# Kernel tuning notes

Measured on AMD Instinct MI355X. Metric: run time of the kernel, lower is better.

The kernel has to match this reference:

```python
import jax, jax.numpy as jnp
import numpy as np
from jax import lax

B, CIN, COUT, H, W = 16, 256, 128, 32, 32
KD = 3   # deformable conv kernel
KU = 4
PAD = 1  # deform conv padding
EPS = 1e-5


def setup_inputs() -> dict:
    key = jax.random.key(0)
    ks = jax.random.split(key, 5)
    s3 = 1.0 / np.sqrt(CIN * KD * KD)
    s_up = 1.0 / np.sqrt(COUT * KU * KU)
    return {
        "x": jax.random.normal(ks[0], (B, CIN, H, W), jnp.float32),
        "w_off": jax.random.normal(ks[1], (3 * KD * KD, CIN, KD, KD), jnp.float32) * s3,
        "b_off": jnp.zeros((3 * KD * KD,), jnp.float32),
        "w_dcn": jax.random.normal(ks[2], (COUT, CIN, KD, KD), jnp.float32) * s3,
        "b_dcn": jnp.zeros((COUT,), jnp.float32),
        "g1": jnp.ones((COUT,), jnp.float32),
        "bt1": jnp.zeros((COUT,), jnp.float32),
        "w_up": jax.random.normal(ks[3], (COUT, COUT, KU, KU), jnp.float32) * s_up,  # torch ConvTranspose2d weight layout (in, out, kh, kw)
        "g2": jnp.ones((COUT,), jnp.float32),
        "bt2": jnp.zeros((COUT,), jnp.float32),
    }


def _conv3x3(x, w, b):
    y = lax.conv_general_dilated(x, w, (1, 1), [(1, 1), (1, 1)],
                                 dimension_numbers=("NCHW", "OIHW", "NCHW"))
    return y + b[None, :, None, None]


def _bn_relu(x, g, b):
    # training-mode BatchNorm2d: batch stats over (N, H, W), biased variance
    mu = jnp.mean(x, (0, 2, 3), keepdims=True)
    var = jnp.var(x, (0, 2, 3), keepdims=True)
    y = (x - mu) * lax.rsqrt(var + EPS)
    return jax.nn.relu(y * g[None, :, None, None] + b[None, :, None, None])


def _deform_conv(x, offset, mask, w, b):
    # modulated deformable conv v2, matching torchvision.ops.DeformConv2d
    Bb, C, Hh, Ww = x.shape
    Kk = KD * KD
    off = offset.reshape(Bb, Kk, 2, Hh, Ww)
    dy, dx = off[:, :, 0], off[:, :, 1]          # [B, Kk, H, W]
    ky, kx = jnp.meshgrid(jnp.arange(KD), jnp.arange(KD), indexing="ij")
    ky = (ky.reshape(-1) - PAD).astype(x.dtype)  # [Kk]
    kx = (kx.reshape(-1) - PAD).astype(x.dtype)
    ii = jnp.arange(Hh, dtype=x.dtype)[None, None, :, None]
    jj = jnp.arange(Ww, dtype=x.dtype)[None, None, None, :]
    py = ii + ky[None, :, None, None] + dy       # [B, Kk, H, W] sample rows
    px = jj + kx[None, :, None, None] + dx       # [B, Kk, H, W] sample cols
    y0 = jnp.floor(py)
    x0 = jnp.floor(px)
    wy = py - y0
    wx = px - x0
    HW = Hh * Ww
    x_flat = x.reshape(Bb, 1, C, HW)

    def corner(yc, xc, wgt):
        valid = (yc >= 0) & (yc <= Hh - 1) & (xc >= 0) & (xc <= Ww - 1)
        yi = jnp.clip(yc, 0, Hh - 1).astype(jnp.int32)
        xi = jnp.clip(xc, 0, Ww - 1).astype(jnp.int32)
        idx = (yi * Ww + xi).reshape(Bb, Kk, 1, HW)
        v = jnp.take_along_axis(x_flat, jnp.broadcast_to(idx, (Bb, Kk, C, HW)), axis=-1)
        wv = (wgt * valid.astype(x.dtype)).reshape(Bb, Kk, 1, HW)
        return v * wv

    samp = (corner(y0, x0, (1 - wy) * (1 - wx)) + corner(y0, x0 + 1, (1 - wy) * wx)
            + corner(y0 + 1, x0, wy * (1 - wx)) + corner(y0 + 1, x0 + 1, wy * wx))
    samp = samp * mask.reshape(Bb, Kk, 1, HW)    # [B, Kk, C, HW]
    out = jnp.einsum("bkcp,ock->bop", samp, w.reshape(w.shape[0], C, Kk))
    return out.reshape(Bb, -1, Hh, Ww) + b[None, :, None, None]


def reference(x, w_off, b_off, w_dcn, b_dcn, g1, bt1, w_up, g2, bt2):
    off = _conv3x3(x, w_off, b_off)              # [B, 27, H, W]
    Kk = KD * KD
    o1, o2, m = off[:, :Kk], off[:, Kk:2 * Kk], off[:, 2 * Kk:]
    offset = jnp.concatenate([o1, o2], axis=1)   # [B, 18, H, W], torchvision pair layout
    mask = jax.nn.sigmoid(m)
    y = _deform_conv(x, offset, mask, w_dcn, b_dcn)
    y = _bn_relu(y, g1, bt1)
    # ConvTranspose2d(k=4, s=2, p=1): conv over lhs-dilated input with flipped kernel
    w_t = jnp.flip(w_up, (2, 3)).transpose(1, 0, 2, 3)  # (out, in, kh, kw)
    p = KU - 1 - 1  # k - 1 - deconv_pad
    y = lax.conv_general_dilated(y, w_t, (1, 1), [(p, p), (p, p)],
                                 lhs_dilation=(2, 2),
                                 dimension_numbers=("NCHW", "OIHW", "NCHW"))
    return _bn_relu(y, g2, bt2)
```

## Files before the change

kernel.cpp:

```cpp
#include <hip/hip_runtime.h>
#include <hip/hip_fp16.h>
#include <math.h>

#define HW 1024
#define EPSV 1e-5f

typedef unsigned int uint;
typedef unsigned short ushort;
typedef __attribute__((ext_vector_type(8))) short short8;
typedef __attribute__((ext_vector_type(8))) _Float16 half8;
typedef __attribute__((ext_vector_type(4))) float floatx4;

static const size_t BOFF = 0;
static const size_t BD   = 36864;
static const size_t BQ   = 184320;
static const size_t XT   = 315392;
static const size_t OFFB = 2412544;
static const size_t ST1  = 2936832;
static const size_t ST2  = 2937856;
static const size_t YP   = 2941952;
static const size_t YSUM = 7136256;
static const size_t YBN  = 8184832;
static const size_t OB   = 9233408;

__device__ inline ushort f2bf(float f) {
  uint u = __builtin_bit_cast(uint, f);
  uint r = (u + 0x7FFFu + ((u >> 16) & 1u)) >> 16;
  return (ushort)r;
}
__device__ inline float b2f(ushort u) {
  return __builtin_bit_cast(float, ((uint)u) << 16);
}

__global__ __launch_bounds__(256) void prep_xt_kernel(const float* __restrict__ x,
                                                      const float* __restrict__ w_off,
                                                      const float* __restrict__ w_dcn,
                                                      const float* __restrict__ w_up,
                                                      float* __restrict__ ws) {
  __shared__ float tile[64 * 65];
  int blk = blockIdx.x;
  int tid = threadIdx.x;
  if (blk < 1024) {
    int b = blk & 15, pt = (blk >> 4) & 15, cc = blk >> 8;
    int p0 = pt * 64, c0 = cc * 64;
    int pp4 = tid & 15, ci = tid >> 4;
#pragma unroll
    for (int it = 0; it < 4; ++it) {
      int c = it * 16 + ci;
      float4 v = *(const float4*)(x + ((size_t)(b * 256 + c0 + c)) * HW + p0 + pp4 * 4);
      tile[c * 65 + pp4 * 4 + 0] = v.x;
      tile[c * 65 + pp4 * 4 + 1] = v.y;
      tile[c * 65 + pp4 * 4 + 2] = v.z;
      tile[c * 65 + pp4 * 4 + 3] = v.w;
    }
    __syncthreads();
    int cp = tid & 31, pp2 = tid >> 5;
    uint* xtu = (uint*)(ws + XT);
#pragma unroll
    for (int it = 0; it < 8; ++it) {
      int p = it * 8 + pp2;
      __half2 h = __floats2half2_rn(tile[(2 * cp) * 65 + p], tile[(2 * cp + 1) * 65 + p]);
      xtu[(size_t)(b * 1024 + p0 + p) * 128 + cc * 32 + cp] = __builtin_bit_cast(uint, h);
    }
  } else if (blk < 3488) {
    int i = (blk - 1024) * 256 + tid;
    if (i < 73728) {
      int c = i & 255; int n = (i >> 8) & 31; int tap = i >> 13;
      float v = (n < 27) ? w_off[((size_t)n * 256 + c) * 9 + tap] : 0.f;
      ((__half*)(ws + BOFF))[i] = __float2half(v);
    } else if (i < 73728 + 294912) {
      int d = i - 73728;
      int oc = d / 2304; int k = d % 2304;
      int tap = k >> 8; int c = k & 255;
      ((__half*)(ws + BD))[d] = __float2half(w_dcn[((size_t)oc * 256 + c) * 9 + tap]);
    } else if (i < 73728 + 294912 + 262144) {
      int d = i - (73728 + 294912);
      int j = d & 7; int n = (d >> 3) & 127; int quad = (d >> 10) & 3;
      int kstep = (d >> 12) & 15; int par = d >> 16;
      int k = kstep * 32 + quad * 8 + j;
      int t4 = k >> 7; int c = k & 127;
      int ty = t4 >> 1, tx = t4 & 1;
      int pu = par >> 1, pv = par & 1;
      int ky = (1 - pu) + 2 * ty, kx = (1 - pv) + 2 * tx;
      float v = w_up[((size_t)c * 128 + n) * 16 + ky * 4 + kx];
      ((ushort*)(ws + BQ))[d] = f2bf(v);
    }
  } else {
    int i = (blk - 3488) * 256 + tid;
    if (i < 5120) ws[ST1 + i] = 0.f;
    else if (i < 5120 + 524288) ws[OFFB + (i - 5120)] = 0.f;
  }
}

__global__ __launch_bounds__(256) void offconv_mfma_kernel(const __half* __restrict__ xt,
                                                           const __half* __restrict__ boff,
                                                           float* __restrict__ off) {
  __shared__ short As[32 * 132];
  __shared__ short Bs[32 * 132];
  int blk = blockIdx.x;
  int b = blk & 15, cs = (blk >> 4) & 1, pt = blk >> 5;
  int P0 = pt * 32;
  int tid = threadIdx.x;
  int wid = tid >> 6, lane = tid & 63, lr = lane & 15, quad = lane >> 4;
  int m_w = (wid & 1) * 16, n_w = (wid >> 1) * 16;
  int arow = tid >> 3, aseg = tid & 7;
  int pix = P0 + arow; int h = pix >> 5, w = pix & 31;

  floatx4 acc = (floatx4)0.f;

  for (int tap = 0; tap < 9; ++tap) {
    int ty = tap / 3, tx = tap % 3;
    int yy = h + ty - 1, xx = w + tx - 1;
    bool valid = (yy >= 0) && (yy < 32) && (xx >= 0) && (xx < 32);
    int pos = min(max(yy, 0), 31) * 32 + min(max(xx, 0), 31);
    const float4* ga = (const float4*)(xt + ((size_t)(b * 1024 + pos)) * 256 + cs * 128 + aseg * 16);
    float4 a0 = ga[0], a1 = ga[1];
    if (!valid) { a0 = make_float4(0.f, 0.f, 0.f, 0.f); a1 = a0; }
    const float4* gb = (const float4*)(boff + ((size_t)(tap * 32 + arow)) * 256 + cs * 128 + aseg * 16);
    float4 b0 = gb[0], b1 = gb[1];
    if (tap) __syncthreads();
    float4* qa = (float4*)(As + arow * 132 + aseg * 16);
    qa[0] = a0; qa[1] = a1;
    float4* qb = (float4*)(Bs + arow * 132 + aseg * 16);
    qb[0] = b0; qb[1] = b1;
    __syncthreads();
#pragma unroll
    for (int k2 = 0; k2 < 4; ++k2) {
      half8 af = *(const half8*)(As + (m_w + lr) * 132 + k2 * 32 + quad * 8);
      half8 bf = *(const half8*)(Bs + (n_w + lr) * 132 + k2 * 32 + quad * 8);
      acc = __builtin_amdgcn_mfma_f32_16x16x32_f16(af, bf, acc, 0, 0, 0);
    }
  }
  int n = n_w + lr;
#pragma unroll
  for (int r = 0; r < 4; ++r) {
    int m = m_w + quad * 4 + r;
    atomicAdd(&off[((size_t)(b * 1024 + P0 + m)) * 32 + n], acc[r]);
  }
}

__global__ __launch_bounds__(256) void deform_mfma_kernel(const __half* __restrict__ xt,
                                                          const float* __restrict__ off,
                                                          const float* __restrict__ b_off,
                                                          const __half* __restrict__ bd,
                                                          ushort* __restrict__ y_part) {
  __shared__ short As[64 * 72];
  __shared__ short Bs[128 * 72];
  int blk = blockIdx.x;
  int b = blk & 15;
  int rr = blk >> 4;
  int ptile = rr & 15, cs = rr >> 4;
  int tid = threadIdx.x;
  int wid = tid >> 6, lane = tid & 63, lr = lane & 15, quad = lane >> 4;
  int m_w = (wid & 1) * 32, n_w = (wid >> 1) * 64;
  int P0 = ptile * 64;
  int pix_l = tid >> 2, cseg = tid & 3;
  int pix = P0 + pix_l;
  int h = pix >> 5, w = pix & 31;
  const float* offb = off + (size_t)(b * 1024 + pix) * 32;
  const __half* xb = xt + (size_t)b * 1024 * 256 + cs * 64 + cseg * 16;
  int ocb = tid >> 1, seg = tid & 1;
  const __half* bdr = bd + (size_t)ocb * 2304 + cs * 64 + seg * 32;

  float4 o4[7];
#pragma unroll
  for (int i = 0; i < 7; ++i) o4[i] = ((const float4*)offb)[i];
  float oflat[28];
#pragma unroll
  for (int i = 0; i < 7; ++i) {
    oflat[4 * i] = o4[i].x; oflat[4 * i + 1] = o4[i].y;
    oflat[4 * i + 2] = o4[i].z; oflat[4 * i + 3] = o4[i].w;
  }

  floatx4 acc[2][4];
#pragma unroll
  for (int mi = 0; mi < 2; ++mi)
#pragma unroll
    for (int ni = 0; ni < 4; ++ni) acc[mi][ni] = (floatx4)0.f;

#pragma unroll
  for (int tap = 0; tap < 9; ++tap) {
    float dy = oflat[2 * tap] + b_off[2 * tap];
    float dx = oflat[2 * tap + 1] + b_off[2 * tap + 1];
    float mraw = oflat[18 + tap] + b_off[18 + tap];
    float mm = 1.f / (1.f + __expf(-mraw));
    float py = (float)(h + tap / 3 - 1) + dy;
    float px = (float)(w + tap % 3 - 1) + dx;
    float y0f = floorf(py), x0f = floorf(px);
    float wy = py - y0f, wx = px - x0f;
    int y0 = (int)y0f, x0 = (int)x0f;
    float cw[4] = {(1.f - wy) * (1.f - wx), (1.f - wy) * wx, wy * (1.f - wx), wy * wx};
    uint4 q[4][2];
    __half2 w2[4];
#pragma unroll
    for (int t = 0; t < 4; ++t) {
      int yy = y0 + (t >> 1), xx = x0 + (t & 1);
      bool v = (yy >= 0) && (yy <= 31) && (xx >= 0) && (xx <= 31);
      int yc = min(max(yy, 0), 31), xc = min(max(xx, 0), 31);
      const uint4* xr = (const uint4*)(xb + (size_t)(yc * 32 + xc) * 256);
      q[t][0] = xr[0]; q[t][1] = xr[1];
      w2[t] = __float2half2_rn(v ? cw[t] * mm : 0.f);
    }
    const float4* gb = (const float4*)(bdr + tap * 256);
    float4 b0 = gb[0], b1 = gb[1], b2 = gb[2], b3 = gb[3];

    __half2 hacc[8];
#pragma unroll
    for (int j = 0; j < 8; ++j) hacc[j] = __float2half2_rn(0.f);
#pragma unroll
    for (int t = 0; t < 4; ++t) {
      uint qa[8] = {q[t][0].x, q[t][0].y, q[t][0].z, q[t][0].w,
                    q[t][1].x, q[t][1].y, q[t][1].z, q[t][1].w};
#pragma unroll
      for (int j = 0; j < 8; ++j)
        hacc[j] = __hfma2(w2[t], __builtin_bit_cast(__half2, qa[j]), hacc[j]);
    }
    if (tap) __syncthreads();
    {
      float4 f0, f1;
      f0.x = __builtin_bit_cast(float, hacc[0]);
      f0.y = __builtin_bit_cast(float, hacc[1]);
      f0.z = __builtin_bit_cast(float, hacc[2]);
      f0.w = __builtin_bit_cast(float, hacc[3]);
      f1.x = __builtin_bit_cast(float, hacc[4]);
      f1.y = __builtin_bit_cast(float, hacc[5]);
      f1.z = __builtin_bit_cast(float, hacc[6]);
      f1.w = __builtin_bit_cast(float, hacc[7]);
      float4* qa2 = (float4*)(As + pix_l * 72 + cseg * 16);
      qa2[0] = f0; qa2[1] = f1;
    }
    float4* qb = (float4*)(Bs + ocb * 72 + seg * 32);
    qb[0] = b0; qb[1] = b1; qb[2] = b2; qb[3] = b3;
    __syncthreads();
#pragma unroll
    for (int k2 = 0; k2 < 2; ++k2) {
      half8 af[2], bf[4];
#pragma unroll
      for (int mi = 0; mi < 2; ++mi)
        af[mi] = *(const half8*)(As + (m_w + mi * 16 + lr) * 72 + k2 * 32 + quad * 8);
#pragma unroll
      for (int ni = 0; ni < 4; ++ni)
        bf[ni] = *(const half8*)(Bs + (n_w + ni * 16 + lr) * 72 + k2 * 32 + quad * 8);
#pragma unroll
      for (int mi = 0; mi < 2; ++mi)
#pragma unroll
        for (int ni = 0; ni < 4; ++ni)
          acc[mi][ni] = __builtin_amdgcn_mfma_f32_16x16x32_f16(af[mi], bf[ni], acc[mi][ni], 0, 0, 0);
    }
  }
  ushort* yp = y_part + (size_t)cs * 2097152 + ((size_t)(b * 1024 + P0)) * 128;
#pragma unroll
  for (int mi = 0; mi < 2; ++mi) {
#pragma unroll
    for (int r = 0; r < 4; ++r) {
      int m = m_w + mi * 16 + quad * 4 + r;
      ushort* orow = yp + (size_t)m * 128;
#pragma unroll
      for (int ni = 0; ni < 4; ++ni)
        orow[n_w + ni * 16 + lr] = f2bf(acc[mi][ni][r]);
    }
  }
}

__global__ __launch_bounds__(256) void yred_kernel(const ushort* __restrict__ yp,
                                                   const float* __restrict__ b_dcn,
                                                   ushort* __restrict__ ysum,
                                                   float* __restrict__ st1) {
  int blk = blockIdx.x;
  int b = blk & 15, seg = blk >> 4;
  int tid = threadIdx.x;
  int px = tid >> 4, ocg = tid & 15;
  int lane = tid & 63, wid = tid >> 6;
  size_t idx = ((size_t)(b * 1024 + seg * 16 + px)) * 128 + ocg * 8;
  short8 p0 = *(const short8*)(yp + idx);
  short8 p1 = *(const short8*)(yp + 2097152 + idx);
  short8 p2 = *(const short8*)(yp + 4194304 + idx);
  short8 p3 = *(const short8*)(yp + 6291456 + idx);
  float s[8], q[8];
  short8 ov;
#pragma unroll
  for (int j = 0; j < 8; ++j) {
    float v = b2f((ushort)p0[j]) + b2f((ushort)p1[j]) + b2f((ushort)p2[j])
            + b2f((ushort)p3[j]) + b_dcn[ocg * 8 + j];
    ov[j] = (short)f2bf(v);
    s[j] = v; q[j] = v * v;
  }
  *(short8*)(ysum + idx) = ov;
#pragma unroll
  for (int j = 0; j < 8; ++j) {
    s[j] += __shfl_xor(s[j], 16); s[j] += __shfl_xor(s[j], 32);
    q[j] += __shfl_xor(q[j], 16); q[j] += __shfl_xor(q[j], 32);
  }
  __shared__ float red[4][256];
  if (lane < 16) {
#pragma unroll
    for (int j = 0; j < 8; ++j) {
      red[wid][lane * 8 + j] = s[j];
      red[wid][128 + lane * 8 + j] = q[j];
    }
  }
  __syncthreads();
  float tot = red[0][tid] + red[1][tid] + red[2][tid] + red[3][tid];
  atomicAdd(&st1[(blk & 3) * 256 + tid], tot);
}

__global__ __launch_bounds__(256) void ybn_kernel(const ushort* __restrict__ ysum,
                                                  const float* __restrict__ st1,
                                                  const float* __restrict__ g1,
                                                  const float* __restrict__ bt1,
                                                  ushort* __restrict__ ybn) {
  __shared__ float scs[128], shs[128];
  int tid = threadIdx.x;
  if (tid < 128) {
    float s  = st1[tid] + st1[256 + tid] + st1[512 + tid] + st1[768 + tid];
    float sq = st1[128 + tid] + st1[384 + tid] + st1[640 + tid] + st1[896 + tid];
    float mean = s / 16384.f;
    float var = sq / 16384.f - mean * mean;
    float sc = g1[tid] * rsqrtf(var + EPSV);
    scs[tid] = sc;
    shs[tid] = fmaf(-mean, sc, bt1[tid]);
  }
  __syncthreads();
  int blk = blockIdx.x;
  int b = blk & 15, seg = blk >> 4;
  int i8 = (b * 64 + seg) * 256 + tid;
  size_t i = (size_t)i8 * 8;
  int oc = (int)(i & 127);
  uint4 pv = *(const uint4*)(ysum + i);
  uint words[4] = {pv.x, pv.y, pv.z, pv.w};
  uint owords[4];
#pragma unroll
  for (int j = 0; j < 4; ++j) {
    ushort u0 = (ushort)(words[j] & 0xFFFFu);
    ushort u1 = (ushort)(words[j] >> 16);
    int c0 = oc + 2 * j, c1 = oc + 2 * j + 1;
    float v0 = fmaxf(fmaf(b2f(u0), scs[c0], shs[c0]), 0.f);
    float v1 = fmaxf(fmaf(b2f(u1), scs[c1], shs[c1]), 0.f);
    owords[j] = (uint)f2bf(v0) | ((uint)f2bf(v1) << 16);
  }
  *(uint4*)(ybn + i) = make_uint4(owords[0], owords[1], owords[2], owords[3]);
}

__global__ __launch_bounds__(256) void deconv_mfma_kernel(const ushort* __restrict__ ybn,
                                                          const ushort* __restrict__ bq,
                                                          ushort* __restrict__ O,
                                                          float* __restrict__ st2) {
  __shared__ short Asd[102 * 132];
  int blk = blockIdx.x;
  int b = blk & 15, par = (blk >> 4) & 3, pt = blk >> 6;
  int pu = par >> 1, pv = par & 1;
  int tid = threadIdx.x;
  int wid = tid >> 6, lane = tid & 63, lr = lane & 15, quad = lane >> 4;
  int P0 = pt * 64;
  int h0 = pt * 2;
  const ushort* ybb = ybn + (size_t)b * 1024 * 128;

  for (int idx = tid; idx < 1632; idx += 256) {
    int pos = idx >> 4, seg = idx & 15;
    int r = pos / 34, jj = pos - r * 34;
    int ig = min(max(h0 + pu - 1 + r, 0), 31);
    int jg = min(max(pv - 1 + jj, 0), 31);
    const float4* src = (const float4*)(ybb + (size_t)(ig * 32 + jg) * 128 + seg * 8);
    *(float4*)(Asd + pos * 132 + seg * 8) = *src;
  }
  __syncthreads();

  int hh[4], ww[4];
#pragma unroll
  for (int mi = 0; mi < 4; ++mi) {
    int p = P0 + mi * 16 + lr;
    hh[mi] = p >> 5; ww[mi] = p & 31;
  }

  floatx4 acc[4][2];
#pragma unroll
  for (int mi = 0; mi < 4; ++mi)
#pragma unroll
    for (int ni = 0; ni < 2; ++ni) acc[mi][ni] = (floatx4)0.f;

  const ushort* bqb = bq + par * 65536 + quad * 1024 + (wid * 32 + lr) * 8;

#pragma unroll
  for (int tap = 0; tap < 4; ++tap) {
    int ty = tap >> 1, tx = tap & 1;
    int apos[4]; bool val[4];
#pragma unroll
    for (int mi = 0; mi < 4; ++mi) {
      int i = hh[mi] + pu - ty, j = ww[mi] + pv - tx;
      val[mi] = (i >= 0) && (i <= 31) && (j >= 0) && (j <= 31);
      int r = hh[mi] - h0 + 1 - ty;
      int jdx = ww[mi] - tx + 1;
      apos[mi] = (r * 34 + jdx) * 132;
    }
#pragma unroll
    for (int k2 = 0; k2 < 4; ++k2) {
      int kstep = tap * 4 + k2;
      int c0 = k2 * 32 + quad * 8;
      short8 bf[2];
#pragma unroll
      for (int ni = 0; ni < 2; ++ni)
        bf[ni] = *(const short8*)(bqb + kstep * 4096 + ni * 128);
      short8 af[4];
#pragma unroll
      for (int mi = 0; mi < 4; ++mi) {
        short8 a = *(const short8*)(Asd + apos[mi] + c0);
        af[mi] = val[mi] ? a : (short8)0;
      }
#pragma unroll
      for (int mi = 0; mi < 4; ++mi)
#pragma unroll
        for (int ni = 0; ni < 2; ++ni)
          acc[mi][ni] = __builtin_amdgcn_mfma_f32_16x16x32_bf16(af[mi], bf[ni], acc[mi][ni], 0, 0, 0);
    }
  }
  size_t obase = (size_t)(b * 4 + par) * 1024 * 128;
#pragma unroll
  for (int mi = 0; mi < 4; ++mi) {
#pragma unroll
    for (int r = 0; r < 4; ++r) {
      int m = mi * 16 + quad * 4 + r;
      ushort* orow = O + obase + (size_t)(P0 + m) * 128 + wid * 32;
#pragma unroll
      for (int ni = 0; ni < 2; ++ni)
        orow[ni * 16 + lr] = f2bf(acc[mi][ni][r]);
    }
  }
  float sn[2], qn[2];
#pragma unroll
  for (int ni = 0; ni < 2; ++ni) {
    float s = 0.f, q = 0.f;
#pragma unroll
    for (int mi = 0; mi < 4; ++mi)
#pragma unroll
      for (int r = 0; r < 4; ++r) {
        float v = acc[mi][ni][r];
        s += v; q = fmaf(v, v, q);
      }
    sn[ni] = s; qn[ni] = q;
  }
#pragma unroll
  for (int ni = 0; ni < 2; ++ni) {
    sn[ni] += __shfl_xor(sn[ni], 16);
    sn[ni] += __shfl_xor(sn[ni], 32);
    qn[ni] += __shfl_xor(qn[ni], 16);
    qn[ni] += __shfl_xor(qn[ni], 32);
  }
  if (lane < 16) {
    float* dst = st2 + pt * 256;
#pragma unroll
    for (int ni = 0; ni < 2; ++ni) {
      atomicAdd(&dst[wid * 32 + ni * 16 + lr], sn[ni]);
      atomicAdd(&dst[128 + wid * 32 + ni * 16 + lr], qn[ni]);
    }
  }
}

__global__ __launch_bounds__(256) void bnout_kernel(const ushort* __restrict__ O,
                                                    const float* __restrict__ st2,
                                                    const float* __restrict__ g2,
                                                    const float* __restrict__ bt2,
                                                    float* __restrict__ out) {
  __shared__ float tile[128 * 65];
  __shared__ float scs[128], shs[128];
  int blk = blockIdx.x;
  int b = blk & 15, pu = (blk >> 4) & 1, uu = blk >> 5;
  int tid = threadIdx.x;
  if (tid < 128) {
    float s = 0.f, sq = 0.f;
#pragma unroll
    for (int c = 0; c < 16; ++c) {
      s += st2[c * 256 + tid];
      sq += st2[c * 256 + 128 + tid];
    }
    float mean = s / 65536.f;
    float var = sq / 65536.f - mean * mean;
    float sc = g2[tid] * rsqrtf(var + EPSV);
    scs[tid] = sc;
    shs[tid] = fmaf(-mean, sc, bt2[tid]);
  }
  __syncthreads();
#pragma unroll
  for (int it = 0; it < 8; ++it) {
    int linear = it * 256 + tid;
    int ocg = linear & 31;
    int vv = (linear >> 5) & 31;
    int pv = linear >> 10;
    const ushort* src = O + ((size_t)(b * 4 + 2 * pu + pv) * 1024 + uu * 32 + vv) * 128 + ocg * 4;
    uint2 u = *(const uint2*)src;
    int col = 2 * vv + pv;
    int oc0 = ocg * 4;
    ushort e0 = (ushort)(u.x & 0xFFFFu), e1 = (ushort)(u.x >> 16);
    ushort e2 = (ushort)(u.y & 0xFFFFu), e3 = (ushort)(u.y >> 16);
    tile[(oc0 + 0) * 65 + col] = fmaxf(fmaf(b2f(e0), scs[oc0 + 0], shs[oc0 + 0]), 0.f);
    tile[(oc0 + 1) * 65 + col] = fmaxf(fmaf(b2f(e1), scs[oc0 + 1], shs[oc0 + 1]), 0.f);
    tile[(oc0 + 2) * 65 + col] = fmaxf(fmaf(b2f(e2), scs[oc0 + 2], shs[oc0 + 2]), 0.f);
    tile[(oc0 + 3) * 65 + col] = fmaxf(fmaf(b2f(e3), scs[oc0 + 3], shs[oc0 + 3]), 0.f);
  }
  __syncthreads();
  int row = 2 * uu + pu;
#pragma unroll
  for (int it = 0; it < 8; ++it) {
    int oc = it * 16 + (tid >> 4);
    int c4 = (tid & 15) * 4;
    float4 v;
    v.x = tile[oc * 65 + c4 + 0];
    v.y = tile[oc * 65 + c4 + 1];
    v.z = tile[oc * 65 + c4 + 2];
    v.w = tile[oc * 65 + c4 + 3];
    *(float4*)(out + ((size_t)(b * 128 + oc)) * 4096 + row * 64 + c4) = v;
  }
}

extern "C" void kernel_launch(void* const* d_in, const int* in_sizes, int n_in,
                              void* d_out, int out_size, void* d_ws, size_t ws_size,
                              hipStream_t stream) {
  const float* x     = (const float*)d_in[0];
  const float* w_off = (const float*)d_in[1];
  const float* b_off = (const float*)d_in[2];
  const float* w_dcn = (const float*)d_in[3];
  const float* b_dcn = (const float*)d_in[4];
  const float* g1    = (const float*)d_in[5];
  const float* bt1   = (const float*)d_in[6];
  const float* w_up  = (const float*)d_in[7];
  const float* g2    = (const float*)d_in[8];
  const float* bt2   = (const float*)d_in[9];
  float* ws  = (float*)d_ws;
  float* out = (float*)d_out;

  prep_xt_kernel<<<5556, 256, 0, stream>>>(x, w_off, w_dcn, w_up, ws);
  offconv_mfma_kernel<<<1024, 256, 0, stream>>>((const __half*)(ws + XT),
                                                (const __half*)(ws + BOFF), ws + OFFB);
  deform_mfma_kernel<<<1024, 256, 0, stream>>>((const __half*)(ws + XT), ws + OFFB, b_off,
                                               (const __half*)(ws + BD), (ushort*)(ws + YP));
  yred_kernel<<<1024, 256, 0, stream>>>((const ushort*)(ws + YP), b_dcn,
                                        (ushort*)(ws + YSUM), ws + ST1);
  ybn_kernel<<<1024, 256, 0, stream>>>((const ushort*)(ws + YSUM), ws + ST1, g1, bt1,
                                       (ushort*)(ws + YBN));
  deconv_mfma_kernel<<<1024, 256, 0, stream>>>((const ushort*)(ws + YBN),
                                               (const ushort*)(ws + BQ),
                                               (ushort*)(ws + OB), ws + ST2);
  bnout_kernel<<<1024, 256, 0, stream>>>((const ushort*)(ws + OB), ws + ST2, g2, bt2, out);
}
```

Before: 169.3 us.

## Fuse BN1+ReLU into deconv staging and restructure offset conv to halo-tile LDS

Drops the separate ybn kernel: the deconv kernel now computes BN1 scale/shift from the accumulated stats and applies normalisation and ReLU while staging its input tile into shared memory. This removes one launch and a full write and read of the normalised activation. The offset conv now loads one image row plus a halo into LDS once, reuses it across all nine taps, and reads pre-swizzled weights straight from global memory in MFMA fragment order. That replaces nine per-tap global loads and barriers. In exchange, BN math is recomputed for overlapping halo elements, and each block stages a larger LDS tile.

```diff
diff --git a/kernel.cpp b/kernel.cpp
--- a/kernel.cpp
+++ b/kernel.cpp
@@ -65,7 +65,14 @@
   } else if (blk < 3488) {
     int i = (blk - 1024) * 256 + tid;
     if (i < 73728) {
-      int c = i & 255; int n = (i >> 8) & 31; int tap = i >> 13;
+      int j = i & 7;
+      int lane = (i >> 3) & 63;
+      int nh = (i >> 9) & 1;
+      int k2 = (i >> 10) & 3;
+      int cs = (i >> 12) & 1;
+      int tap = i >> 13;
+      int n = nh * 16 + (lane & 15);
+      int c = cs * 128 + k2 * 32 + (lane >> 4) * 8 + j;
       float v = (n < 27) ? w_off[((size_t)n * 256 + c) * 9 + tap] : 0.f;
       ((__half*)(ws + BOFF))[i] = __float2half(v);
     } else if (i < 73728 + 294912) {
@@ -93,49 +100,50 @@
 }
 
 __global__ __launch_bounds__(256) void offconv_mfma_kernel(const __half* __restrict__ xt,
-                                                           const __half* __restrict__ boff,
+                                                           const __half* __restrict__ bofr,
                                                            float* __restrict__ off) {
-  __shared__ short As[32 * 132];
-  __shared__ short Bs[32 * 132];
+  __shared__ short As[102 * 132];
   int blk = blockIdx.x;
   int b = blk & 15, cs = (blk >> 4) & 1, pt = blk >> 5;
-  int P0 = pt * 32;
+  int h = pt;
   int tid = threadIdx.x;
   int wid = tid >> 6, lane = tid & 63, lr = lane & 15, quad = lane >> 4;
-  int m_w = (wid & 1) * 16, n_w = (wid >> 1) * 16;
-  int arow = tid >> 3, aseg = tid & 7;
-  int pix = P0 + arow; int h = pix >> 5, w = pix & 31;
+  int m_w = (wid & 1) * 16, nh = wid >> 1;
+  int n_w = nh * 16;
+  const __half* xb = xt + (size_t)b * 1024 * 256 + cs * 128;
+
+  for (int idx = tid; idx < 1632; idx += 256) {
+    int pos = idx >> 4, seg = idx & 15;
+    int r = pos / 34, jj = pos - r * 34;
+    int ig = min(max(h - 1 + r, 0), 31);
+    int jg = min(max(jj - 1, 0), 31);
+    const float4* src = (const float4*)(xb + (size_t)(ig * 32 + jg) * 256 + seg * 8);
+    *(float4*)(As + pos * 132 + seg * 8) = *src;
+  }
+  __syncthreads();
 
   floatx4 acc = (floatx4)0.f;
-
+  int m = m_w + lr;
+  const __half* bb = bofr + (size_t)lane * 8;
+#pragma unroll
   for (int tap = 0; tap < 9; ++tap) {
     int ty = tap / 3, tx = tap % 3;
-    int yy = h + ty - 1, xx = w + tx - 1;
-    bool valid = (yy >= 0) && (yy < 32) && (xx >= 0) && (xx < 32);
-    int pos = min(max(yy, 0), 31) * 32 + min(max(xx, 0), 31);
-    const float4* ga = (const float4*)(xt + ((size_t)(b * 1024 + pos)) * 256 + cs * 128 + aseg * 16);
-    float4 a0 = ga[0], a1 = ga[1];
-    if (!valid) { a0 = make_float4(0.f, 0.f, 0.f, 0.f); a1 = a0; }
-    const float4* gb = (const float4*)(boff + ((size_t)(tap * 32 + arow)) * 256 + cs * 128 + aseg * 16);
-    float4 b0 = gb[0], b1 = gb[1];
-    if (tap) __syncthreads();
-    float4* qa = (float4*)(As + arow * 132 + aseg * 16);
-    qa[0] = a0; qa[1] = a1;
-    float4* qb = (float4*)(Bs + arow * 132 + aseg * 16);
-    qb[0] = b0; qb[1] = b1;
-    __syncthreads();
+    bool valid = (h + ty - 1 >= 0) && (h + ty - 1 <= 31) && (m + tx - 1 >= 0) && (m + tx - 1 <= 31);
+    int apos = (ty * 34 + m + tx) * 132;
 #pragma unroll
     for (int k2 = 0; k2 < 4; ++k2) {
-      half8 af = *(const half8*)(As + (m_w + lr) * 132 + k2 * 32 + quad * 8);
-      half8 bf = *(const half8*)(Bs + (n_w + lr) * 132 + k2 * 32 + quad * 8);
+      short8 a = *(const short8*)(As + apos + k2 * 32 + quad * 8);
+      short8 az = valid ? a : (short8)0;
+      half8 af = __builtin_bit_cast(half8, az);
+      half8 bf = *(const half8*)(bb + (size_t)((((tap * 2 + cs) * 4 + k2) * 2) + nh) * 512);
       acc = __builtin_amdgcn_mfma_f32_16x16x32_f16(af, bf, acc, 0, 0, 0);
     }
   }
   int n = n_w + lr;
 #pragma unroll
   for (int r = 0; r < 4; ++r) {
-    int m = m_w + quad * 4 + r;
-    atomicAdd(&off[((size_t)(b * 1024 + P0 + m)) * 32 + n], acc[r]);
+    int mm = m_w + quad * 4 + r;
+    atomicAdd(&off[((size_t)(b * 1024 + pt * 32 + mm)) * 32 + n], acc[r]);
   }
 }
 
@@ -304,13 +312,24 @@
   atomicAdd(&st1[(blk & 3) * 256 + tid], tot);
 }
 
-__global__ __launch_bounds__(256) void ybn_kernel(const ushort* __restrict__ ysum,
-                                                  const float* __restrict__ st1,
-                                                  const float* __restrict__ g1,
-                                                  const float* __restrict__ bt1,
-                                                  ushort* __restrict__ ybn) {
+__global__ __launch_bounds__(256) void deconv_mfma_kernel(const ushort* __restrict__ ysum,
+                                                          const float* __restrict__ st1,
+                                                          const float* __restrict__ g1,
+                                                          const float* __restrict__ bt1,
+                                                          const ushort* __restrict__ bq,
+                                                          ushort* __restrict__ O,
+                                                          float* __restrict__ st2) {
+  __shared__ short Asd[102 * 132];
   __shared__ float scs[128], shs[128];
+  int blk = blockIdx.x;
+  int b = blk & 15, par = (blk >> 4) & 3, pt = blk >> 6;
+  int pu = par >> 1, pv = par & 1;
   int tid = threadIdx.x;
+  int wid = tid >> 6, lane = tid & 63, lr = lane & 15, quad = lane >> 4;
+  int P0 = pt * 64;
+  int h0 = pt * 2;
+  const ushort* ysb = ysum + (size_t)b * 1024 * 128;
+
   if (tid < 128) {
     float s  = st1[tid] + st1[256 + tid] + st1[512 + tid] + st1[768 + tid];
     float sq = st1[128 + tid] + st1[384 + tid] + st1[640 + tid] + st1[896 + tid];
@@ -321,47 +340,27 @@
     shs[tid] = fmaf(-mean, sc, bt1[tid]);
   }
   __syncthreads();
-  int blk = blockIdx.x;
-  int b = blk & 15, seg = blk >> 4;
-  int i8 = (b * 64 + seg) * 256 + tid;
-  size_t i = (size_t)i8 * 8;
-  int oc = (int)(i & 127);
-  uint4 pv = *(const uint4*)(ysum + i);
-  uint words[4] = {pv.x, pv.y, pv.z, pv.w};
-  uint owords[4];
-#pragma unroll
-  for (int j = 0; j < 4; ++j) {
-    ushort u0 = (ushort)(words[j] & 0xFFFFu);
-    ushort u1 = (ushort)(words[j] >> 16);
-    int c0 = oc + 2 * j, c1 = oc + 2 * j + 1;
-    float v0 = fmaxf(fmaf(b2f(u0), scs[c0], shs[c0]), 0.f);
-    float v1 = fmaxf(fmaf(b2f(u1), scs[c1], shs[c1]), 0.f);
-    owords[j] = (uint)f2bf(v0) | ((uint)f2bf(v1) << 16);
-  }
-  *(uint4*)(ybn + i) = make_uint4(owords[0], owords[1], owords[2], owords[3]);
-}
-
-__global__ __launch_bounds__(256) void deconv_mfma_kernel(const ushort* __restrict__ ybn,
-                                                          const ushort* __restrict__ bq,
-                                                          ushort* __restrict__ O,
-                                                          float* __restrict__ st2) {
-  __shared__ short Asd[102 * 132];
-  int blk = blockIdx.x;
-  int b = blk & 15, par = (blk >> 4) & 3, pt = blk >> 6;
-  int pu = par >> 1, pv = par & 1;
-  int tid = threadIdx.x;
-  int wid = tid >> 6, lane = tid & 63, lr = lane & 15, quad = lane >> 4;
-  int P0 = pt * 64;
-  int h0 = pt * 2;
-  const ushort* ybb = ybn + (size_t)b * 1024 * 128;
 
   for (int idx = tid; idx < 1632; idx += 256) {
     int pos = idx >> 4, seg = idx & 15;
     int r = pos / 34, jj = pos - r * 34;
     int ig = min(max(h0 + pu - 1 + r, 0), 31);
     int jg = min(max(pv - 1 + jj, 0), 31);
-    const float4* src = (const float4*)(ybb + (size_t)(ig * 32 + jg) * 128 + seg * 8);
-    *(float4*)(Asd + pos * 132 + seg * 8) = *src;
+    uint4 u = *(const uint4*)(ysb + (size_t)(ig * 32 + jg) * 128 + seg * 8);
+    uint words[4] = {u.x, u.y, u.z, u.w};
+    uint ow[4];
+    int oc0 = seg * 8;
+#pragma unroll
+    for (int j = 0; j < 4; ++j) {
+      ushort u0 = (ushort)(words[j] & 0xFFFFu);
+      ushort u1 = (ushort)(words[j] >> 16);
+      int c0 = oc0 + 2 * j, c1 = oc0 + 2 * j + 1;
+      float v0 = fmaxf(fmaf(b2f(u0), scs[c0], shs[c0]), 0.f);
+      float v1 = fmaxf(fmaf(b2f(u1), scs[c1], shs[c1]), 0.f);
+      ow[j] = (uint)f2bf(v0) | ((uint)f2bf(v1) << 16);
+    }
+    uint4 packed = make_uint4(ow[0], ow[1], ow[2], ow[3]);
+    *(uint4*)(Asd + pos * 132 + seg * 8) = packed;
   }
   __syncthreads();
 
@@ -534,9 +533,7 @@
                                                (const __half*)(ws + BD), (ushort*)(ws + YP));
   yred_kernel<<<1024, 256, 0, stream>>>((const ushort*)(ws + YP), b_dcn,
                                         (ushort*)(ws + YSUM), ws + ST1);
-  ybn_kernel<<<1024, 256, 0, stream>>>((const ushort*)(ws + YSUM), ws + ST1, g1, bt1,
-                                       (ushort*)(ws + YBN));
-  deconv_mfma_kernel<<<1024, 256, 0, stream>>>((const ushort*)(ws + YBN),
+  deconv_mfma_kernel<<<1024, 256, 0, stream>>>((const ushort*)(ws + YSUM), ws + ST1, g1, bt1,
                                                (const ushort*)(ws + BQ),
                                                (ushort*)(ws + OB), ws + ST2);
   bnout_kernel<<<1024, 256, 0, stream>>>((const ushort*)(ws + OB), ws + ST2, g2, bt2, out);
```

After: 160.0 us (median of 2 runs). 5.4% less time.
